# Kernel optimization log

Measured on AMD Instinct MI355X. Metric: run time of the kernel, lower is better.

## Reference

```python
import jax, jax.numpy as jnp
import numpy as np

H = 4           # LSTM hidden size
T = 200         # seq len (T * H == 800, required by the reshape)
FEAT = 800      # flattened feature size into the linear
OUT = 28        # linear output dim


def run_lstm_layer(x, Wih, Whh, bih, bhh):
    """Single LSTM layer, PyTorch gate order (i, f, g, o). x: [B, T, I] -> [B, T, H]."""
    B = x.shape[0]
    xT = jnp.swapaxes(x, 0, 1)  # [T, B, I]
    h0 = jnp.zeros((B, H), x.dtype)
    c0 = jnp.zeros((B, H), x.dtype)
    b = bih + bhh  # [4H]

    def step(carry, xt):
        h, c = carry
        gates = xt @ Wih.T + h @ Whh.T + b  # [B, 4H]
        i, f, g, o = jnp.split(gates, 4, axis=-1)
        i = jax.nn.sigmoid(i)
        f = jax.nn.sigmoid(f)
        g = jnp.tanh(g)
        o = jax.nn.sigmoid(o)
        c = f * c + i * g
        h = o * jnp.tanh(c)
        return (h, c), h

    _, hs = jax.lax.scan(step, (h0, c0), xT)  # hs: [T, B, H]
    return jnp.swapaxes(hs, 0, 1)  # [B, T, H]


def setup_inputs() -> dict:
    key = jax.random.key(0)
    ks = jax.random.split(key, 12)
    B, I = 32768, 4
    s_lstm = 1.0 / np.sqrt(H)     # torch LSTM init bound
    s_lin = 1.0 / np.sqrt(FEAT)   # torch Linear init bound

    def u(k, shape, s):
        return jax.random.uniform(k, shape, jnp.float32, -s, s)

    return {
        "x": jax.random.normal(ks[0], (B, T, I), jnp.float32),
        "Wih0": u(ks[1], (4 * H, I), s_lstm),
        "Whh0": u(ks[2], (4 * H, H), s_lstm),
        "bih0": u(ks[3], (4 * H,), s_lstm),
        "bhh0": u(ks[4], (4 * H,), s_lstm),
        "Wih1": u(ks[5], (4 * H, H), s_lstm),
        "Whh1": u(ks[6], (4 * H, H), s_lstm),
        "bih1": u(ks[7], (4 * H,), s_lstm),
        "bhh1": u(ks[8], (4 * H,), s_lstm),
        "Wout": u(ks[9], (OUT, FEAT), s_lin),
        "bout": u(ks[10], (OUT,), s_lin),
    }


def reference(x, Wih0, Whh0, bih0, bhh0, Wih1, Whh1, bih1, bhh1, Wout, bout):
    h1 = run_lstm_layer(x, Wih0, Whh0, bih0, bhh0)   # [B, T, H]
    h2 = run_lstm_layer(h1, Wih1, Whh1, bih1, bhh1)  # [B, T, H]
    feat = h2.reshape(-1, FEAT)                      # [B, 800] since T*H == 800
    return feat @ Wout.T + bout                      # [B, 28]
```

## Files before the change

### kernel.cpp

```cpp
#include <hip/hip_runtime.h>

#define T_STEPS 200
#define OUTD 28

typedef float f2 __attribute__((ext_vector_type(2)));

template<int SRC>
__device__ __forceinline__ float qb(float v) {
    return __int_as_float(__builtin_amdgcn_update_dpp(
        0, __float_as_int(v), SRC * 0x55, 0xF, 0xF, true));
}

#define PIN2(v) asm volatile("" : "+v"(v))
#define PINF(v) asm volatile("" : "+v"(v))

__global__ void transpose_wout(const float* __restrict__ Wout, float* __restrict__ Wt) {
    int idx = blockIdx.x * 256 + threadIdx.x;
    if (idx < T_STEPS * OUTD * 4) {
        int t = idx / (OUTD * 4);
        int r = idx - t * (OUTD * 4);
        int j = r >> 2, c = r & 3;
        Wt[idx] = Wout[j * 800 + 4 * t + c];
    }
}

__device__ __forceinline__ void layer_step(const f2 (&wia)[4], const f2 (&wib)[4],
                                           const f2 (&wha)[4], const f2 (&whb)[4],
                                           const f2 (&bb)[4],
                                           f2 ina, f2 inb,
                                           f2& ha, f2& hb, float& c)
{
    float g[4];
#pragma unroll
    for (int gi = 0; gi < 4; ++gi) {
        f2 s = bb[gi];
        s += wia[gi] * ina;
        s += wib[gi] * inb;
        s += wha[gi] * ha;
        s += whb[gi] * hb;
        g[gi] = s.x + s.y;
    }
    float Ei = __builtin_amdgcn_exp2f(g[0]);
    float Ef = __builtin_amdgcn_exp2f(g[1]);
    float Eg = __builtin_amdgcn_exp2f(g[2]);
    float Eo = __builtin_amdgcn_exp2f(g[3]);
    float Ai = 1.0f + Ei, Af = 1.0f + Ef, Ag = 1.0f + Eg, Ao = 1.0f + Eo;
    float P   = Ai * Ag;
    float num = c * P + (Eg - 1.0f) * Af;
    c = num * __builtin_amdgcn_rcpf(P * Af);
    float cc = fminf(fmaxf(c, -16.0f), 16.0f);
    float Ec = __builtin_amdgcn_exp2f(2.8853900817779268f * cc);
    float ho = (Ec - 1.0f) * __builtin_amdgcn_rcpf(Ao * (1.0f + Ec));
    ha = f2{qb<0>(ho), qb<1>(ho)};
    hb = f2{qb<2>(ho), qb<3>(ho)};
}

template<bool PREF>
__device__ __forceinline__ void full_step(
    const f2 (&wi0a)[4], const f2 (&wi0b)[4], const f2 (&wh0a)[4], const f2 (&wh0b)[4],
    const f2 (&wi1a)[4], const f2 (&wi1b)[4], const f2 (&wh1a)[4], const f2 (&wh1b)[4],
    const f2 (&b0)[4], const f2 (&b1)[4],
    f2& h1a0, f2& h1b0, f2& h2a0, f2& h2b0, float& c10, float& c20,
    f2& h1a1, f2& h1b1, f2& h2a1, f2& h2b1, float& c11, float& c21,
    f2 (&acc0)[7], f2 (&acc1)[7],
    float4& xs0, float4& xs1,
    const char* xp, unsigned xo0, unsigned xo1, int tpf,
    const char* wtp, unsigned w_off)
{
    float4 wo[7];
#pragma unroll
    for (int jj = 0; jj < 7; ++jj)
        wo[jj] = *(const float4*)(wtp + w_off + jj * 16);

    f2 xa0 = f2{xs0.x, xs0.y}, xb0 = f2{xs0.z, xs0.w};
    f2 xa1 = f2{xs1.x, xs1.y}, xb1 = f2{xs1.z, xs1.w};

    layer_step(wi0a, wi0b, wh0a, wh0b, b0, xa0, xb0, h1a0, h1b0, c10);
    layer_step(wi0a, wi0b, wh0a, wh0b, b0, xa1, xb1, h1a1, h1b1, c11);

    if (PREF) {
        xs0 = *(const float4*)(xp + xo0 + (size_t)tpf * 16);
        xs1 = *(const float4*)(xp + xo1 + (size_t)tpf * 16);
    }

    layer_step(wi1a, wi1b, wh1a, wh1b, b1, h1a0, h1b0, h2a0, h2b0, c20);
    layer_step(wi1a, wi1b, wh1a, wh1b, b1, h1a1, h1b1, h2a1, h2b1, c21);

#pragma unroll
    for (int jj = 0; jj < 7; ++jj) {
        f2 wa = f2{wo[jj].x, wo[jj].y};
        f2 wb = f2{wo[jj].z, wo[jj].w};
        acc0[jj] += wa * h2a0; acc0[jj] += wb * h2b0;
        acc1[jj] += wa * h2a1; acc1[jj] += wb * h2b1;
    }
}

__global__ __launch_bounds__(256)
__attribute__((amdgpu_waves_per_eu(1, 1)))
void lstm2_fused(const float* __restrict__ x,
                 const float* __restrict__ Wih0, const float* __restrict__ Whh0,
                 const float* __restrict__ bih0, const float* __restrict__ bhh0,
                 const float* __restrict__ Wih1, const float* __restrict__ Whh1,
                 const float* __restrict__ bih1, const float* __restrict__ bhh1,
                 const float* __restrict__ Wt,   const float* __restrict__ bout,
                 float* __restrict__ out, int batch)
{
    const int tid = blockIdx.x * 256 + threadIdx.x;
    const int quad = tid >> 2;
    const int k = tid & 3;
    const int e0 = quad * 2, e1 = e0 + 1;
    if (e1 >= batch) return;

    f2 wi0a[4], wi0b[4], wh0a[4], wh0b[4];
    f2 wi1a[4], wi1b[4], wh1a[4], wh1b[4];
    f2 b0[4], b1[4];
#pragma unroll
    for (int gi = 0; gi < 4; ++gi) {
        const int row = gi * 4 + k;
        const float sc = (gi == 2) ? 2.8853900817779268f : -1.4426950408889634f;
        float4 a = ((const float4*)Wih0)[row];
        float4 c = ((const float4*)Whh0)[row];
        float4 d = ((const float4*)Wih1)[row];
        float4 e = ((const float4*)Whh1)[row];
        wi0a[gi] = f2{a.x * sc, a.y * sc}; wi0b[gi] = f2{a.z * sc, a.w * sc};
        wh0a[gi] = f2{c.x * sc, c.y * sc}; wh0b[gi] = f2{c.z * sc, c.w * sc};
        wi1a[gi] = f2{d.x * sc, d.y * sc}; wi1b[gi] = f2{d.z * sc, d.w * sc};
        wh1a[gi] = f2{e.x * sc, e.y * sc}; wh1b[gi] = f2{e.z * sc, e.w * sc};
        b0[gi] = f2{(bih0[row] + bhh0[row]) * sc, 0.0f};
        b1[gi] = f2{(bih1[row] + bhh1[row]) * sc, 0.0f};
    }
#pragma unroll
    for (int gi = 0; gi < 4; ++gi) {
        PIN2(wi0a[gi]); PIN2(wi0b[gi]); PIN2(wh0a[gi]); PIN2(wh0b[gi]);
        PIN2(wi1a[gi]); PIN2(wi1b[gi]); PIN2(wh1a[gi]); PIN2(wh1b[gi]);
        PIN2(b0[gi]);   PIN2(b1[gi]);
    }

    f2 acc0[7], acc1[7];
#pragma unroll
    for (int jj = 0; jj < 7; ++jj) {
        float bj = bout[k * 7 + jj];
        acc0[jj] = f2{bj, 0.0f};
        acc1[jj] = f2{bj, 0.0f};
    }

    f2 h1a0 = f2{0,0}, h1b0 = f2{0,0}, h2a0 = f2{0,0}, h2b0 = f2{0,0};
    f2 h1a1 = f2{0,0}, h1b1 = f2{0,0}, h2a1 = f2{0,0}, h2b1 = f2{0,0};
    float c10 = 0.0f, c20 = 0.0f, c11 = 0.0f, c21 = 0.0f;

    const char* xp  = (const char*)x;
    const unsigned xo0 = (unsigned)e0 * 3200u;
    const unsigned xo1 = (unsigned)e1 * 3200u;
    const char* wtp = (const char*)Wt;
    const unsigned w_off = (unsigned)k * 112u;

    float4 xv0 = *(const float4*)(xp + xo0);
    float4 xv1 = *(const float4*)(xp + xo1);
    float4 xn0 = *(const float4*)(xp + xo0 + 16);
    float4 xn1 = *(const float4*)(xp + xo1 + 16);

    for (int t = 0; t < T_STEPS - 2; t += 2) {
        full_step<true>(wi0a, wi0b, wh0a, wh0b, wi1a, wi1b, wh1a, wh1b, b0, b1,
                        h1a0, h1b0, h2a0, h2b0, c10, c20,
                        h1a1, h1b1, h2a1, h2b1, c11, c21,
                        acc0, acc1, xv0, xv1, xp, xo0, xo1, t + 2, wtp, w_off);
        wtp += OUTD * 16;
        full_step<true>(wi0a, wi0b, wh0a, wh0b, wi1a, wi1b, wh1a, wh1b, b0, b1,
                        h1a0, h1b0, h2a0, h2b0, c10, c20,
                        h1a1, h1b1, h2a1, h2b1, c11, c21,
                        acc0, acc1, xn0, xn1, xp, xo0, xo1, t + 3, wtp, w_off);
        wtp += OUTD * 16;
    }
    full_step<false>(wi0a, wi0b, wh0a, wh0b, wi1a, wi1b, wh1a, wh1b, b0, b1,
                     h1a0, h1b0, h2a0, h2b0, c10, c20,
                     h1a1, h1b1, h2a1, h2b1, c11, c21,
                     acc0, acc1, xv0, xv1, xp, xo0, xo1, 0, wtp, w_off);
    wtp += OUTD * 16;
    full_step<false>(wi0a, wi0b, wh0a, wh0b, wi1a, wi1b, wh1a, wh1b, b0, b1,
                     h1a0, h1b0, h2a0, h2b0, c10, c20,
                     h1a1, h1b1, h2a1, h2b1, c11, c21,
                     acc0, acc1, xn0, xn1, xp, xo0, xo1, 0, wtp, w_off);

    float* op0 = out + (size_t)e0 * OUTD + k * 7;
    float* op1 = out + (size_t)e1 * OUTD + k * 7;
#pragma unroll
    for (int jj = 0; jj < 7; ++jj) {
        op0[jj] = acc0[jj].x + acc0[jj].y;
        op1[jj] = acc1[jj].x + acc1[jj].y;
    }
}

extern "C" void kernel_launch(void* const* d_in, const int* in_sizes, int n_in,
                              void* d_out, int out_size, void* d_ws, size_t ws_size,
                              hipStream_t stream) {
    const float* x    = (const float*)d_in[0];
    const float* Wih0 = (const float*)d_in[1];
    const float* Whh0 = (const float*)d_in[2];
    const float* bih0 = (const float*)d_in[3];
    const float* bhh0 = (const float*)d_in[4];
    const float* Wih1 = (const float*)d_in[5];
    const float* Whh1 = (const float*)d_in[6];
    const float* bih1 = (const float*)d_in[7];
    const float* bhh1 = (const float*)d_in[8];
    const float* Wout = (const float*)d_in[9];
    const float* bout = (const float*)d_in[10];
    float* out = (float*)d_out;
    float* Wt  = (float*)d_ws;

    transpose_wout<<<(T_STEPS * OUTD * 4 + 255) / 256, 256, 0, stream>>>(Wout, Wt);

    const int batch = in_sizes[0] / (T_STEPS * 4);
    const int threads = (batch / 2) * 4;
    const int grid = threads / 256;
    lstm2_fused<<<grid, 256, 0, stream>>>(
        x, Wih0, Whh0, bih0, bhh0, Wih1, Whh1, bih1, bhh1, Wt, bout, out, batch);
}
```

Measured before the change: 234.7 us.

## Software-pipeline LSTM layers so layer 0 step t+1 overlaps layer 1 step t

Restructures the time loop into a skewed pipeline. Each iteration computes layer 0 at step t+1 alongside layer 1 at step t, using double-buffered layer-0 hidden states (A/B sets), with a prologue and an epilogue. This breaks the serial dependency between the two layers within an iteration, giving the scheduler independent work to hide exp/rcp/DPP latency. The cost is more live registers at one wave per EU and more complex prologue/epilogue indexing.

New measurement: 264.5 us. 1.13x slower.

```diff
diff --git a/kernel.cpp b/kernel.cpp
--- a/kernel.cpp
+++ b/kernel.cpp
@@ -12,7 +12,6 @@
 }
 
 #define PIN2(v) asm volatile("" : "+v"(v))
-#define PINF(v) asm volatile("" : "+v"(v))
 
 __global__ void transpose_wout(const float* __restrict__ Wout, float* __restrict__ Wt) {
     int idx = blockIdx.x * 256 + threadIdx.x;
@@ -28,7 +27,8 @@
                                            const f2 (&wha)[4], const f2 (&whb)[4],
                                            const f2 (&bb)[4],
                                            f2 ina, f2 inb,
-                                           f2& ha, f2& hb, float& c)
+                                           f2 hin_a, f2 hin_b,
+                                           f2& hout_a, f2& hout_b, float& c)
 {
     float g[4];
 #pragma unroll
@@ -36,8 +36,8 @@
         f2 s = bb[gi];
         s += wia[gi] * ina;
         s += wib[gi] * inb;
-        s += wha[gi] * ha;
-        s += whb[gi] * hb;
+        s += wha[gi] * hin_a;
+        s += whb[gi] * hin_b;
         g[gi] = s.x + s.y;
     }
     float Ei = __builtin_amdgcn_exp2f(g[0]);
@@ -51,17 +51,19 @@
     float cc = fminf(fmaxf(c, -16.0f), 16.0f);
     float Ec = __builtin_amdgcn_exp2f(2.8853900817779268f * cc);
     float ho = (Ec - 1.0f) * __builtin_amdgcn_rcpf(Ao * (1.0f + Ec));
-    ha = f2{qb<0>(ho), qb<1>(ho)};
-    hb = f2{qb<2>(ho), qb<3>(ho)};
+    hout_a = f2{qb<0>(ho), qb<1>(ho)};
+    hout_b = f2{qb<2>(ho), qb<3>(ho)};
 }
 
 template<bool PREF>
-__device__ __forceinline__ void full_step(
+__device__ __forceinline__ void pipe_step(
     const f2 (&wi0a)[4], const f2 (&wi0b)[4], const f2 (&wh0a)[4], const f2 (&wh0b)[4],
     const f2 (&wi1a)[4], const f2 (&wi1b)[4], const f2 (&wh1a)[4], const f2 (&wh1b)[4],
     const f2 (&b0)[4], const f2 (&b1)[4],
-    f2& h1a0, f2& h1b0, f2& h2a0, f2& h2b0, float& c10, float& c20,
-    f2& h1a1, f2& h1b1, f2& h2a1, f2& h2b1, float& c11, float& c21,
+    f2& p1a0, f2& p1b0, f2& p1a1, f2& p1b1,
+    f2& q1a0, f2& q1b0, f2& q1a1, f2& q1b1,
+    float& c10, float& c11,
+    f2& h2a0, f2& h2b0, f2& h2a1, f2& h2b1, float& c20, float& c21,
     f2 (&acc0)[7], f2 (&acc1)[7],
     float4& xs0, float4& xs1,
     const char* xp, unsigned xo0, unsigned xo1, int tpf,
@@ -75,16 +77,16 @@
     f2 xa0 = f2{xs0.x, xs0.y}, xb0 = f2{xs0.z, xs0.w};
     f2 xa1 = f2{xs1.x, xs1.y}, xb1 = f2{xs1.z, xs1.w};
 
-    layer_step(wi0a, wi0b, wh0a, wh0b, b0, xa0, xb0, h1a0, h1b0, c10);
-    layer_step(wi0a, wi0b, wh0a, wh0b, b0, xa1, xb1, h1a1, h1b1, c11);
+    layer_step(wi0a, wi0b, wh0a, wh0b, b0, xa0, xb0, p1a0, p1b0, q1a0, q1b0, c10);
+    layer_step(wi0a, wi0b, wh0a, wh0b, b0, xa1, xb1, p1a1, p1b1, q1a1, q1b1, c11);
 
     if (PREF) {
         xs0 = *(const float4*)(xp + xo0 + (size_t)tpf * 16);
         xs1 = *(const float4*)(xp + xo1 + (size_t)tpf * 16);
     }
 
-    layer_step(wi1a, wi1b, wh1a, wh1b, b1, h1a0, h1b0, h2a0, h2b0, c20);
-    layer_step(wi1a, wi1b, wh1a, wh1b, b1, h1a1, h1b1, h2a1, h2b1, c21);
+    layer_step(wi1a, wi1b, wh1a, wh1b, b1, p1a0, p1b0, h2a0, h2b0, h2a0, h2b0, c20);
+    layer_step(wi1a, wi1b, wh1a, wh1b, b1, p1a1, p1b1, h2a1, h2b1, h2a1, h2b1, c21);
 
 #pragma unroll
     for (int jj = 0; jj < 7; ++jj) {
@@ -144,8 +146,9 @@
         acc1[jj] = f2{bj, 0.0f};
     }
 
-    f2 h1a0 = f2{0,0}, h1b0 = f2{0,0}, h2a0 = f2{0,0}, h2b0 = f2{0,0};
-    f2 h1a1 = f2{0,0}, h1b1 = f2{0,0}, h2a1 = f2{0,0}, h2b1 = f2{0,0};
+    f2 h1Aa0 = f2{0,0}, h1Ab0 = f2{0,0}, h1Aa1 = f2{0,0}, h1Ab1 = f2{0,0};
+    f2 h1Ba0 = f2{0,0}, h1Bb0 = f2{0,0}, h1Ba1 = f2{0,0}, h1Bb1 = f2{0,0};
+    f2 h2a0 = f2{0,0}, h2b0 = f2{0,0}, h2a1 = f2{0,0}, h2b1 = f2{0,0};
     float c10 = 0.0f, c20 = 0.0f, c11 = 0.0f, c21 = 0.0f;
 
     const char* xp  = (const char*)x;
@@ -159,27 +162,63 @@
     float4 xn0 = *(const float4*)(xp + xo0 + 16);
     float4 xn1 = *(const float4*)(xp + xo1 + 16);
 
-    for (int t = 0; t < T_STEPS - 2; t += 2) {
-        full_step<true>(wi0a, wi0b, wh0a, wh0b, wi1a, wi1b, wh1a, wh1b, b0, b1,
-                        h1a0, h1b0, h2a0, h2b0, c10, c20,
-                        h1a1, h1b1, h2a1, h2b1, c11, c21,
-                        acc0, acc1, xv0, xv1, xp, xo0, xo1, t + 2, wtp, w_off);
+    {
+        f2 z = f2{0, 0};
+        f2 xa0 = f2{xv0.x, xv0.y}, xb0 = f2{xv0.z, xv0.w};
+        f2 xa1 = f2{xv1.x, xv1.y}, xb1 = f2{xv1.z, xv1.w};
+        layer_step(wi0a, wi0b, wh0a, wh0b, b0, xa0, xb0, z, z, h1Aa0, h1Ab0, c10);
+        layer_step(wi0a, wi0b, wh0a, wh0b, b0, xa1, xb1, z, z, h1Aa1, h1Ab1, c11);
+        xv0 = *(const float4*)(xp + xo0 + 2 * 16);
+        xv1 = *(const float4*)(xp + xo1 + 2 * 16);
+    }
+
+    for (int t = 1; t <= 195; t += 2) {
+        pipe_step<true>(wi0a, wi0b, wh0a, wh0b, wi1a, wi1b, wh1a, wh1b, b0, b1,
+                        h1Aa0, h1Ab0, h1Aa1, h1Ab1,
+                        h1Ba0, h1Bb0, h1Ba1, h1Bb1,
+                        c10, c11, h2a0, h2b0, h2a1, h2b1, c20, c21,
+                        acc0, acc1, xn0, xn1, xp, xo0, xo1, t + 2, wtp, w_off);
         wtp += OUTD * 16;
-        full_step<true>(wi0a, wi0b, wh0a, wh0b, wi1a, wi1b, wh1a, wh1b, b0, b1,
-                        h1a0, h1b0, h2a0, h2b0, c10, c20,
-                        h1a1, h1b1, h2a1, h2b1, c11, c21,
-                        acc0, acc1, xn0, xn1, xp, xo0, xo1, t + 3, wtp, w_off);
+        pipe_step<true>(wi0a, wi0b, wh0a, wh0b, wi1a, wi1b, wh1a, wh1b, b0, b1,
+                        h1Ba0, h1Bb0, h1Ba1, h1Bb1,
+                        h1Aa0, h1Ab0, h1Aa1, h1Ab1,
+                        c10, c11, h2a0, h2b0, h2a1, h2b1, c20, c21,
+                        acc0, acc1, xv0, xv1, xp, xo0, xo1, t + 3, wtp, w_off);
         wtp += OUTD * 16;
     }
-    full_step<false>(wi0a, wi0b, wh0a, wh0b, wi1a, wi1b, wh1a, wh1b, b0, b1,
-                     h1a0, h1b0, h2a0, h2b0, c10, c20,
-                     h1a1, h1b1, h2a1, h2b1, c11, c21,
+    pipe_step<true>(wi0a, wi0b, wh0a, wh0b, wi1a, wi1b, wh1a, wh1b, b0, b1,
+                    h1Aa0, h1Ab0, h1Aa1, h1Ab1,
+                    h1Ba0, h1Bb0, h1Ba1, h1Bb1,
+                    c10, c11, h2a0, h2b0, h2a1, h2b1, c20, c21,
+                    acc0, acc1, xn0, xn1, xp, xo0, xo1, 199, wtp, w_off);
+    wtp += OUTD * 16;
+    pipe_step<false>(wi0a, wi0b, wh0a, wh0b, wi1a, wi1b, wh1a, wh1b, b0, b1,
+                     h1Ba0, h1Bb0, h1Ba1, h1Bb1,
+                     h1Aa0, h1Ab0, h1Aa1, h1Ab1,
+                     c10, c11, h2a0, h2b0, h2a1, h2b1, c20, c21,
                      acc0, acc1, xv0, xv1, xp, xo0, xo1, 0, wtp, w_off);
     wtp += OUTD * 16;
-    full_step<false>(wi0a, wi0b, wh0a, wh0b, wi1a, wi1b, wh1a, wh1b, b0, b1,
-                     h1a0, h1b0, h2a0, h2b0, c10, c20,
-                     h1a1, h1b1, h2a1, h2b1, c11, c21,
+    pipe_step<false>(wi0a, wi0b, wh0a, wh0b, wi1a, wi1b, wh1a, wh1b, b0, b1,
+                     h1Aa0, h1Ab0, h1Aa1, h1Ab1,
+                     h1Ba0, h1Bb0, h1Ba1, h1Bb1,
+                     c10, c11, h2a0, h2b0, h2a1, h2b1, c20, c21,
                      acc0, acc1, xn0, xn1, xp, xo0, xo1, 0, wtp, w_off);
+    wtp += OUTD * 16;
+    {
+        float4 wo[7];
+#pragma unroll
+        for (int jj = 0; jj < 7; ++jj)
+            wo[jj] = *(const float4*)(wtp + w_off + jj * 16);
+        layer_step(wi1a, wi1b, wh1a, wh1b, b1, h1Ba0, h1Bb0, h2a0, h2b0, h2a0, h2b0, c20);
+        layer_step(wi1a, wi1b, wh1a, wh1b, b1, h1Ba1, h1Bb1, h2a1, h2b1, h2a1, h2b1, c21);
+#pragma unroll
+        for (int jj = 0; jj < 7; ++jj) {
+            f2 wa = f2{wo[jj].x, wo[jj].y};
+            f2 wb = f2{wo[jj].z, wo[jj].w};
+            acc0[jj] += wa * h2a0; acc0[jj] += wb * h2b0;
+            acc1[jj] += wa * h2a1; acc1[jj] += wb * h2b1;
+        }
+    }
 
     float* op0 = out + (size_t)e0 * OUTD + k * 7;
     float* op1 = out + (size_t)e1 * OUTD + k * 7;
```
